# Kernel optimization log

Hardware: AMD Instinct MI355X
Metric: run time of the kernel (lower is better)

## Reference

```python
import math
import jax, jax.numpy as jnp
import numpy as np
from jax import lax

B, C, O, K, WDIM, H, W = 8, 512, 512, 3, 512, 64, 64
CONV_SCALE = 1.0 / math.sqrt(C * K * K)
MOD_SCALE = 1.0 / math.sqrt(WDIM)


def setup_inputs() -> dict:
    key = jax.random.key(0)
    k1, k2, k3, k4 = jax.random.split(key, 4)
    return {
        "x": jax.random.normal(k1, (B, C, H, W), dtype=jnp.float32),
        "w": jax.random.normal(k2, (B, WDIM), dtype=jnp.float32),
        "base_weight": jax.random.normal(k3, (1, O, C, K, K), dtype=jnp.float32),
        "mod_weight": jax.random.normal(k4, (C, WDIM), dtype=jnp.float32),
        "mod_bias": jnp.zeros((C,), dtype=jnp.float32),
    }


def reference(x, w, base_weight, mod_weight, mod_bias):
    # EqualLinear modulation: s in (B, C), then +1
    s = w @ (mod_weight * MOD_SCALE).T + mod_bias + 1.0  # (B, C)
    # Per-sample modulated weights: (B, O, C, K, K)
    weight = CONV_SCALE * base_weight * s[:, None, :, None, None]
    # Demodulation
    d = lax.rsqrt(jnp.sum(weight * weight, axis=(2, 3, 4), keepdims=True))
    weight = weight * d
    pad = K // 2

    def conv_one(xi, wi):
        # xi: (C, H, W), wi: (O, C, K, K)
        return lax.conv_general_dilated(
            xi[None], wi, window_strides=(1, 1),
            padding=[(pad, pad), (pad, pad)],
            dimension_numbers=("NCHW", "OIHW", "NCHW"),
        )[0]

    return jax.vmap(conv_one)(x, weight)  # (B, O, H, W)
```

## Files before the change

### kernel.cpp

```cpp
#include <hip/hip_runtime.h>
#include <stdint.h>


#define MOD_SCALE  0.044194173824159216f
#define CONV_SCALE 0.014731391274719739f

typedef __attribute__((ext_vector_type(4))) float f32x4;
typedef __attribute__((ext_vector_type(8))) short bf16x8;

__device__ inline unsigned short f2bf(float f) {
  uint32_t u = __float_as_uint(f);
  uint32_t r = (u + 0x7fffu + ((u >> 16) & 1u)) >> 16;
  return (unsigned short)r;
}

__device__ inline void gload_lds16(const void* g, void* l) {
  __builtin_amdgcn_global_load_lds(
      (const __attribute__((address_space(1))) void*)g,
      (__attribute__((address_space(3))) void*)l, 16, 0, 0);
}

__global__ __launch_bounds__(256) void k_style(const float* __restrict__ w,
                                               const float* __restrict__ modw,
                                               const float* __restrict__ modb,
                                               float* __restrict__ s_out) {
  int idx = blockIdx.x * 256 + threadIdx.x;
  int b = idx >> 9, c = idx & 511;
  const float4* wd = (const float4*)(w + (b << 9));
  const float4* md = (const float4*)(modw + (c << 9));
  float acc = 0.f;
#pragma unroll 8
  for (int i = 0; i < 128; ++i) {
    float4 a = wd[i], m = md[i];
    acc += a.x * m.x + a.y * m.y + a.z * m.z + a.w * m.w;
  }
  s_out[idx] = acc * MOD_SCALE + modb[c] + 1.0f;
}

__global__ __launch_bounds__(256) void k_wsq(const float* __restrict__ bw,
                                             float* __restrict__ wsq) {
  int idx = blockIdx.x * 256 + threadIdx.x;
  const float* p = bw + (size_t)idx * 9;
  float a = 0.f;
#pragma unroll
  for (int k = 0; k < 9; ++k) a += p[k] * p[k];
  wsq[idx] = a;
}

__global__ __launch_bounds__(256) void k_demod(const float* __restrict__ s,
                                               const float* __restrict__ wsq,
                                               float* __restrict__ dd) {
  int gw = (blockIdx.x * 256 + threadIdx.x) >> 6;
  int lane = threadIdx.x & 63;
  int b = gw >> 9, o = gw & 511;
  const float* sp = s + (b << 9);
  const float* wp = wsq + (o << 9);
  float a = 0.f;
#pragma unroll
  for (int t = 0; t < 8; ++t) {
    int c = lane + (t << 6);
    float sv = sp[c];
    a += sv * sv * wp[c];
  }
#pragma unroll
  for (int off = 32; off > 0; off >>= 1) a += __shfl_down(a, off, 64);
  if (lane == 0) dd[gw] = rsqrtf(a * (1.0f / 4608.0f));
}

__global__ __launch_bounds__(256) void k_wmod(const float* __restrict__ bw,
                                              const float* __restrict__ s,
                                              const float* __restrict__ dd,
                                              unsigned short* __restrict__ wm) {
  __shared__ float lw[4608];
  __shared__ float ls[512];
  const int tid = threadIdx.x;
  const int o = blockIdx.x, b = blockIdx.y;
  const float* src = bw + (size_t)o * 4608;
#pragma unroll
  for (int i = 0; i < 18; ++i) lw[tid + (i << 8)] = src[tid + (i << 8)];
  ls[tid] = s[(b << 9) + tid];
  ls[tid + 256] = s[(b << 9) + 256 + tid];
  __syncthreads();
  const float dscale = dd[(b << 9) + o] * CONV_SCALE;
  uint32_t* dst = (uint32_t*)(wm + (size_t)((b << 9) + o) * 4608);
  const int c0 = tid << 1;
  const int base = c0 * 9;
#pragma unroll
  for (int j = 0; j < 9; ++j) {
    float v0 = lw[base + j] * ls[c0] * dscale;
    float v1 = lw[base + 9 + j] * ls[c0 + 1] * dscale;
    dst[(j << 8) + tid] = (uint32_t)f2bf(v0) | ((uint32_t)f2bf(v1) << 16);
  }
}

__global__ __launch_bounds__(256) void k_border(unsigned short* __restrict__ xp) {
  int p = blockIdx.x, b = blockIdx.y;
  int py, px;
  if (p < 66)       { py = 0;       px = p; }
  else if (p < 132) { py = 65;      px = p - 66; }
  else if (p < 196) { py = p - 131; px = 0; }
  else              { py = p - 195; px = 65; }
  uint32_t* dst = (uint32_t*)(xp + ((size_t)b * 4356 + py * 66 + px) * 512);
  dst[threadIdx.x] = 0u;
}

__global__ __launch_bounds__(256) void k_xpose(const float* __restrict__ x,
                                               unsigned short* __restrict__ xp) {
  __shared__ unsigned short tile[64 * 65];
  const int b = blockIdx.z, c0 = blockIdx.y << 6, p0 = blockIdx.x << 6;
  const int tid = threadIdx.x;
  {
    const int pi = tid & 63, ci0 = tid >> 6;
    const float* src = x + (size_t)((b << 9) + c0 + ci0) * 4096 + p0 + pi;
#pragma unroll
    for (int it = 0; it < 16; ++it)
      tile[(ci0 + (it << 2)) * 65 + pi] = f2bf(src[(size_t)(it << 2) * 4096]);
  }
  __syncthreads();
  {
    const int co = tid & 63, po0 = tid >> 6;
#pragma unroll
    for (int it = 0; it < 16; ++it) {
      int p = po0 + (it << 2);
      int gp = p0 + p;
      int py = (gp >> 6) + 1, px = (gp & 63) + 1;
      xp[((size_t)b * 4356 + py * 66 + px) * 512 + c0 + co] = tile[co * 65 + p];
    }
  }
}

__global__ __launch_bounds__(256, 4) void k_conv(const unsigned short* __restrict__ wmodT,
                                                 const unsigned short* __restrict__ xpad,
                                                 float* __restrict__ out) {
  __shared__ alignas(16) unsigned short As[8192];
  __shared__ alignas(16) unsigned short Bs[8192];
  const int tid = threadIdx.x;
  const int b  = blockIdx.z;
  const int m0 = blockIdx.y << 7;
  const int n0 = blockIdx.x << 7;
  const int y0 = n0 >> 6;

  const int srow = tid >> 3;
  const int schk = ((tid & 7) - (srow & 7)) & 7;
  const int scol = schk << 3;

  const unsigned short* Ag = wmodT + (size_t)((b << 9) + m0 + srow) * 4608 + scol;
  const size_t bx = (size_t)b * (66 * 66 * 512);

  const int lane = tid & 63;
  const int wv   = tid >> 6;
  const int moff = (wv >> 1) << 6;
  const int noff = (wv & 1) << 6;
  const int lm   = lane & 15;
  const int g4   = lane >> 4;

  const unsigned short* ardA[2];
  const unsigned short* ardB[2];
#pragma unroll
  for (int h = 0; h < 2; ++h) {
    ardA[h] = As + (moff + lm) * 64 + ((((h << 2) + g4) + moff + lm) & 7) * 8;
    ardB[h] = Bs + (noff + lm) * 64 + ((((h << 2) + g4) + noff + lm) & 7) * 8;
  }

  f32x4 acc[4][4];
#pragma unroll
  for (int i = 0; i < 4; ++i)
#pragma unroll
    for (int j = 0; j < 4; ++j) acc[i][j] = (f32x4){0.f, 0.f, 0.f, 0.f};

#pragma unroll 1
  for (int tap = 0; tap < 9; ++tap) {
    const int ky = (tap * 11) >> 5;
    const int kx = tap - ky * 3;
    const unsigned short* Bt[4];
#pragma unroll
    for (int g = 0; g < 4; ++g) {
      const int n = (g << 5) + srow;
      Bt[g] = xpad + bx +
              (size_t)((y0 + ky + (n >> 6)) * 66 + kx + (n & 63)) * 512 + scol;
    }
#pragma unroll 1
    for (int kb = 0; kb < 8; ++kb) {
#pragma unroll
      for (int g = 0; g < 4; ++g)
        gload_lds16(Ag + g * (32 * 4608), As + (((g << 8) + tid) << 3));
#pragma unroll
      for (int g = 0; g < 4; ++g)
        gload_lds16(Bt[g] + (kb << 6), Bs + (((g << 8) + tid) << 3));
      Ag += 64;
      __syncthreads();
#pragma unroll
      for (int h = 0; h < 2; ++h) {
        bf16x8 af[4], bf[4];
#pragma unroll
        for (int i = 0; i < 4; ++i) af[i] = *(const bf16x8*)(ardA[h] + (i << 10));
#pragma unroll
        for (int j = 0; j < 4; ++j) bf[j] = *(const bf16x8*)(ardB[h] + (j << 10));
#pragma unroll
        for (int i = 0; i < 4; ++i)
#pragma unroll
          for (int j = 0; j < 4; ++j)
            acc[i][j] = __builtin_amdgcn_mfma_f32_16x16x32_bf16(af[i], bf[j], acc[i][j], 0, 0, 0);
      }
      __syncthreads();
    }
  }

  float* op = out + (size_t)((b << 9) + m0 + moff) * 4096 + n0 + noff;
#pragma unroll
  for (int i = 0; i < 4; ++i) {
#pragma unroll
    for (int r = 0; r < 4; ++r) {
      const int m = i * 16 + (g4 << 2) + r;
#pragma unroll
      for (int j = 0; j < 4; ++j)
        op[(size_t)m * 4096 + (j << 4) + lm] = acc[i][j][r];
    }
  }
}

extern "C" void kernel_launch(void* const* d_in, const int* in_sizes, int n_in,
                              void* d_out, int out_size, void* d_ws, size_t ws_size,
                              hipStream_t stream) {
  const float* x    = (const float*)d_in[0];
  const float* w    = (const float*)d_in[1];
  const float* bw   = (const float*)d_in[2];
  const float* modw = (const float*)d_in[3];
  const float* modb = (const float*)d_in[4];
  float* out = (float*)d_out;
  char* ws = (char*)d_ws;

  float* s_buf  = (float*)(ws);
  float* dd_buf = (float*)(ws + 16384);
  float* wsq    = (float*)(ws + 32768);
  unsigned short* wmod = (unsigned short*)(ws + 1081344);
  unsigned short* xpad = (unsigned short*)(ws + 38830080);

  (void)in_sizes; (void)n_in; (void)out_size; (void)ws_size;

  k_style <<<16, 256, 0, stream>>>(w, modw, modb, s_buf);
  k_wsq   <<<1024, 256, 0, stream>>>(bw, wsq);
  k_demod <<<1024, 256, 0, stream>>>(s_buf, wsq, dd_buf);
  k_wmod  <<<dim3(512, 8), 256, 0, stream>>>(bw, s_buf, dd_buf, wmod);
  k_border<<<dim3(260, 8), 256, 0, stream>>>(xpad);
  k_xpose <<<dim3(64, 8, 8), 256, 0, stream>>>(x, xpad);
  k_conv  <<<dim3(32, 4, 8), 256, 0, stream>>>(wmod, xpad, out);
}
```

Before: 313.4 us.

## Fuse weight-square, demod and modulation kernels; parallelize style GEMV

Merges k_wsq, k_demod and k_wmod into a single kernel that loads each output channel's base weight once. It computes per-channel squared sums, reduces the demod factor for all 8 batches in-block, and writes modulated bf16 weights for every batch. The style GEMV now splits each dot product across 4 threads with a shared-memory reduction and launches 64 blocks instead of 16. This removes two launches and the global round-trips through wsq/dd, but the fused kernel runs only 512 blocks, each doing 8 batches serially.

```diff
diff --git a/kernel.cpp b/kernel.cpp
--- a/kernel.cpp
+++ b/kernel.cpp
@@ -24,72 +24,86 @@
                                                const float* __restrict__ modw,
                                                const float* __restrict__ modb,
                                                float* __restrict__ s_out) {
-  int idx = blockIdx.x * 256 + threadIdx.x;
-  int b = idx >> 9, c = idx & 511;
-  const float4* wd = (const float4*)(w + (b << 9));
-  const float4* md = (const float4*)(modw + (c << 9));
+  __shared__ float red[256];
+  const int t = threadIdx.x;
+  const int cb = blockIdx.x, b = blockIdx.y;
+  const int cl = t >> 2, q = t & 3;
+  const int c = (cb << 6) + cl;
+  const float4* wd = (const float4*)(w + (b << 9) + (q << 7));
+  const float4* md = (const float4*)(modw + ((size_t)c << 9) + (q << 7));
   float acc = 0.f;
-#pragma unroll 8
-  for (int i = 0; i < 128; ++i) {
+#pragma unroll
+  for (int i = 0; i < 32; ++i) {
     float4 a = wd[i], m = md[i];
     acc += a.x * m.x + a.y * m.y + a.z * m.z + a.w * m.w;
   }
-  s_out[idx] = acc * MOD_SCALE + modb[c] + 1.0f;
-}
-
-__global__ __launch_bounds__(256) void k_wsq(const float* __restrict__ bw,
-                                             float* __restrict__ wsq) {
-  int idx = blockIdx.x * 256 + threadIdx.x;
-  const float* p = bw + (size_t)idx * 9;
-  float a = 0.f;
-#pragma unroll
-  for (int k = 0; k < 9; ++k) a += p[k] * p[k];
-  wsq[idx] = a;
-}
-
-__global__ __launch_bounds__(256) void k_demod(const float* __restrict__ s,
-                                               const float* __restrict__ wsq,
-                                               float* __restrict__ dd) {
-  int gw = (blockIdx.x * 256 + threadIdx.x) >> 6;
-  int lane = threadIdx.x & 63;
-  int b = gw >> 9, o = gw & 511;
-  const float* sp = s + (b << 9);
-  const float* wp = wsq + (o << 9);
-  float a = 0.f;
-#pragma unroll
-  for (int t = 0; t < 8; ++t) {
-    int c = lane + (t << 6);
-    float sv = sp[c];
-    a += sv * sv * wp[c];
-  }
-#pragma unroll
-  for (int off = 32; off > 0; off >>= 1) a += __shfl_down(a, off, 64);
-  if (lane == 0) dd[gw] = rsqrtf(a * (1.0f / 4608.0f));
-}
-
-__global__ __launch_bounds__(256) void k_wmod(const float* __restrict__ bw,
-                                              const float* __restrict__ s,
-                                              const float* __restrict__ dd,
-                                              unsigned short* __restrict__ wm) {
+  red[t] = acc;
+  __syncthreads();
+  if (t < 64) {
+    float v = red[t * 4] + red[t * 4 + 1] + red[t * 4 + 2] + red[t * 4 + 3];
+    int cc = (cb << 6) + t;
+    s_out[(b << 9) + cc] = v * MOD_SCALE + modb[cc] + 1.0f;
+  }
+}
+
+__global__ __launch_bounds__(256) void k_fw(const float* __restrict__ bw,
+                                            const float* __restrict__ s,
+                                            unsigned short* __restrict__ wm) {
   __shared__ float lw[4608];
-  __shared__ float ls[512];
+  __shared__ float ls[4096];
+  __shared__ float red[32];
+  __shared__ float sc8[8];
   const int tid = threadIdx.x;
-  const int o = blockIdx.x, b = blockIdx.y;
-  const float* src = bw + (size_t)o * 4608;
-#pragma unroll
-  for (int i = 0; i < 18; ++i) lw[tid + (i << 8)] = src[tid + (i << 8)];
-  ls[tid] = s[(b << 9) + tid];
-  ls[tid + 256] = s[(b << 9) + 256 + tid];
-  __syncthreads();
-  const float dscale = dd[(b << 9) + o] * CONV_SCALE;
-  uint32_t* dst = (uint32_t*)(wm + (size_t)((b << 9) + o) * 4608);
+  const int o = blockIdx.x;
+  {
+    const float4* src = (const float4*)(bw + (size_t)o * 4608);
+    float4* dst = (float4*)lw;
+#pragma unroll
+    for (int i = 0; i < 4; ++i) dst[tid + (i << 8)] = src[tid + (i << 8)];
+    if (tid < 128) dst[tid + 1024] = src[tid + 1024];
+  }
+  {
+    const float4* src = (const float4*)s;
+    float4* dst = (float4*)ls;
+#pragma unroll
+    for (int i = 0; i < 4; ++i) dst[tid + (i << 8)] = src[tid + (i << 8)];
+  }
+  __syncthreads();
   const int c0 = tid << 1;
   const int base = c0 * 9;
+  float wq0 = 0.f, wq1 = 0.f;
 #pragma unroll
   for (int j = 0; j < 9; ++j) {
-    float v0 = lw[base + j] * ls[c0] * dscale;
-    float v1 = lw[base + 9 + j] * ls[c0 + 1] * dscale;
-    dst[(j << 8) + tid] = (uint32_t)f2bf(v0) | ((uint32_t)f2bf(v1) << 16);
+    float a = lw[base + j];     wq0 += a * a;
+    float b2 = lw[base + 9 + j]; wq1 += b2 * b2;
+  }
+  const int lane = tid & 63, wv = tid >> 6;
+#pragma unroll
+  for (int b = 0; b < 8; ++b) {
+    float s0 = ls[(b << 9) + c0], s1 = ls[(b << 9) + c0 + 1];
+    float v = wq0 * s0 * s0 + wq1 * s1 * s1;
+#pragma unroll
+    for (int off = 32; off > 0; off >>= 1) v += __shfl_down(v, off, 64);
+    if (lane == 0) red[(b << 2) + wv] = v;
+  }
+  __syncthreads();
+  if (tid < 8) {
+    float a = red[tid << 2] + red[(tid << 2) + 1] + red[(tid << 2) + 2] + red[(tid << 2) + 3];
+    sc8[tid] = rsqrtf(a * (1.0f / 4608.0f)) * CONV_SCALE;
+  }
+  __syncthreads();
+#pragma unroll 1
+  for (int b = 0; b < 8; ++b) {
+    const float dsc = sc8[b];
+    const float s0 = ls[(b << 9) + c0] * dsc;
+    const float s1 = ls[(b << 9) + c0 + 1] * dsc;
+    uint32_t* dst = (uint32_t*)(wm + (size_t)((b << 9) + o) * 4608);
+#pragma unroll
+    for (int j = 0; j < 9; ++j) {
+      float v0 = lw[base + j] * s0;
+      float v1 = lw[base + 9 + j] * s1;
+      dst[(j << 8) + tid] = (uint32_t)f2bf(v0) | ((uint32_t)f2bf(v1) << 16);
+    }
   }
 }
 
@@ -230,18 +244,14 @@
   float* out = (float*)d_out;
   char* ws = (char*)d_ws;
 
-  float* s_buf  = (float*)(ws);
-  float* dd_buf = (float*)(ws + 16384);
-  float* wsq    = (float*)(ws + 32768);
-  unsigned short* wmod = (unsigned short*)(ws + 1081344);
-  unsigned short* xpad = (unsigned short*)(ws + 38830080);
+  float* s_buf = (float*)(ws);
+  unsigned short* wmod = (unsigned short*)(ws + 16384);
+  unsigned short* xpad = (unsigned short*)(ws + 37765120);
 
   (void)in_sizes; (void)n_in; (void)out_size; (void)ws_size;
 
-  k_style <<<16, 256, 0, stream>>>(w, modw, modb, s_buf);
-  k_wsq   <<<1024, 256, 0, stream>>>(bw, wsq);
-  k_demod <<<1024, 256, 0, stream>>>(s_buf, wsq, dd_buf);
-  k_wmod  <<<dim3(512, 8), 256, 0, stream>>>(bw, s_buf, dd_buf, wmod);
+  k_style <<<dim3(8, 8), 256, 0, stream>>>(w, modw, modb, s_buf);
+  k_fw    <<<512, 256, 0, stream>>>(bw, s_buf, wmod);
   k_border<<<dim3(260, 8), 256, 0, stream>>>(xpad);
   k_xpose <<<dim3(64, 8, 8), 256, 0, stream>>>(x, xpad);
   k_conv  <<<dim3(32, 4, 8), 256, 0, stream>>>(wmod, xpad, out);
```

New measurement: 301.2 us. 1.04x faster.
